# Optimization experiments

Measured on AMD Instinct MI355X. Metric: run time of the kernel, lower is better.

The kernel has to match this reference:

```python
import jax, jax.numpy as jnp
import numpy as np

H, D = 2, 128            # heads, per-head dim
F_OUT = H * D            # out_channels = 256
N_ADD = 20000
N_DEL = 20000
E = 200000
N_SEL = 4096


def setup_inputs() -> dict:
    key = jax.random.key(0)
    ks = jax.random.split(key, 24)
    p = lambda k, shp: (jax.random.normal(k, shp, dtype=jnp.float32) * 0.05)
    inp = {
        "x_add": jax.random.normal(ks[0], (N_ADD, 768), dtype=jnp.float32),
        "x_del": jax.random.normal(ks[1], (N_DEL, 768), dtype=jnp.float32),
        # per-node-type projections (torch Linear: W [out,in], b [out])
        "W_add": p(ks[2], (F_OUT, 768)), "b_add": p(ks[3], (F_OUT,)),
        "W_del": p(ks[4], (F_OUT, 768)), "b_del": p(ks[5], (F_OUT,)),
        # per-edge-type attention vectors [H, D]
        "att_ad_s": p(ks[6], (H, D)), "att_ad_d": p(ks[7], (H, D)),
        "att_da_s": p(ks[8], (H, D)), "att_da_d": p(ks[9], (H, D)),
        "att_aa_s": p(ks[10], (H, D)), "att_aa_d": p(ks[11], (H, D)),
        "att_dd_s": p(ks[12], (H, D)), "att_dd_d": p(ks[13], (H, D)),
        # semantic attention: k_lin Linear(F_OUT->F_OUT) and query q [F_OUT]
        "k_W": p(ks[14], (F_OUT, F_OUT)), "k_b": p(ks[15], (F_OUT,)),
        "q": p(ks[16], (F_OUT,)),
        # edge indices: row 0 = src node ids, row 1 = dst node ids
        "ei_ad": jax.random.randint(ks[17], (2, E), 0, N_ADD),
        "ei_da": jax.random.randint(ks[18], (2, E), 0, N_DEL),
        "ei_aa": jax.random.randint(ks[19], (2, E), 0, N_ADD),
        "ei_dd": jax.random.randint(ks[20], (2, E), 0, N_DEL),
        "del_idx": jax.random.randint(ks[21], (N_SEL,), 0, N_DEL),
    }
    return inp


def _seg_softmax(a, seg, n):
    # numerically-stable softmax over edges grouped by destination node
    m = jax.ops.segment_max(a, seg, num_segments=n)
    m = jnp.where(jnp.isfinite(m), m, 0.0)
    e = jnp.exp(a - m[seg])
    s = jax.ops.segment_sum(e, seg, num_segments=n)
    return e / (s[seg] + 1e-16)


def _edge_attn(x_src, x_dst, att_s, att_d, ei, n_dst):
    # x_*: [N, H, D]; GAT-style additive attention with leaky_relu(0.2)
    a_s = (x_src * att_s).sum(-1)                   # [Ns, H]
    a_d = (x_dst * att_d).sum(-1)                   # [Nd, H]
    alpha = jax.nn.leaky_relu(a_s[ei[0]] + a_d[ei[1]], 0.2)  # [E, H]
    alpha = _seg_softmax(alpha, ei[1], n_dst)       # [E, H]
    msg = x_src[ei[0]] * alpha[:, :, None]          # [E, H, D]
    out = jax.ops.segment_sum(msg, ei[1], num_segments=n_dst)  # [Nd, H, D]
    return jax.nn.relu(out).reshape(n_dst, F_OUT)


def _group(xs, q, k_W, k_b):
    # semantic (metapath-level) attention
    out = jnp.stack(xs)                              # [M, N, F]
    score = (q * jnp.tanh(out @ k_W.T + k_b).mean(axis=1)).sum(-1)  # [M]
    attn = jax.nn.softmax(score)
    return (attn[:, None, None] * out).sum(0)        # [N, F]


def reference(x_add, x_del, W_add, b_add, W_del, b_del,
              att_ad_s, att_ad_d, att_da_s, att_da_d,
              att_aa_s, att_aa_d, att_dd_s, att_dd_d,
              k_W, k_b, q, ei_ad, ei_da, ei_aa, ei_dd, del_idx):
    ha = (x_add @ W_add.T + b_add).reshape(N_ADD, H, D)
    hd = (x_del @ W_del.T + b_del).reshape(N_DEL, H, D)
    # messages grouped by destination node type
    out_del_ad = _edge_attn(ha, hd, att_ad_s, att_ad_d, ei_ad, N_DEL)
    out_del_dd = _edge_attn(hd, hd, att_dd_s, att_dd_d, ei_dd, N_DEL)
    out_add_da = _edge_attn(hd, ha, att_da_s, att_da_d, ei_da, N_ADD)
    out_add_aa = _edge_attn(ha, ha, att_aa_s, att_aa_d, ei_aa, N_ADD)
    out_del = _group([out_del_ad, out_del_dd], q, k_W, k_b)
    _ = _group([out_add_da, out_add_aa], q, k_W, k_b)  # computed by HANConv, unused downstream
    return out_del[del_idx]  # index_select on del_node
```

## Files before the change

kernel.cpp:

```cpp
#include <hip/hip_runtime.h>
#include <hip/hip_bf16.h>


typedef unsigned short u16;
typedef __attribute__((ext_vector_type(8))) __bf16 bf16x8;
typedef __attribute__((ext_vector_type(4))) float f32x4;
typedef const __attribute__((address_space(1))) unsigned int* gu32p;
typedef __attribute__((address_space(3))) unsigned int* su32p;

#define CAP 48

__device__ inline float bf2f(u16 u) {
    union { unsigned int i; float f; } c; c.i = ((unsigned int)u) << 16; return c.f;
}
__device__ inline u16 f2bf(float f) {
    union { float f; unsigned int i; } c; c.f = f;
    return (u16)((c.i + 0x7fffu + ((c.i >> 16) & 1u)) >> 16);
}
__device__ inline bf16x8 cvt8(f32x4 a, f32x4 b) {
    bf16x8 r;
    r[0] = (__bf16)a[0]; r[1] = (__bf16)a[1]; r[2] = (__bf16)a[2]; r[3] = (__bf16)a[3];
    r[4] = (__bf16)b[0]; r[5] = (__bf16)b[1]; r[6] = (__bf16)b[2]; r[7] = (__bf16)b[3];
    return r;
}
__device__ inline float fast_tanh(float x) {
    x = fminf(9.f, fmaxf(-9.f, x));
    float t = __expf(2.f * x);
    return (t - 1.f) / (t + 1.f);
}

__global__ __launch_bounds__(256) void prep_fill(const float* __restrict__ W0, u16* __restrict__ wb0,
                                                 const float* __restrict__ W1, u16* __restrict__ wb1,
                                                 const float* __restrict__ kW, u16* __restrict__ kwb,
                                                 const int* __restrict__ eiA, int* __restrict__ cntA,
                                                 int* __restrict__ srcsA,
                                                 const int* __restrict__ eiB, int* __restrict__ cntB,
                                                 int* __restrict__ srcsB, int E) {
    int b = blockIdx.x;
    if (b < 224) {
        int idx = b * 256 + threadIdx.x;
        const float* s; u16* d; int i;
        if (idx < 24576)      { s = W0; d = wb0; i = idx; }
        else if (idx < 49152) { s = W1; d = wb1; i = idx - 24576; }
        else                  { s = kW; d = kwb; i = idx - 49152; }
        int e = i * 8;
        *(bf16x8*)(d + e) = cvt8(*(const f32x4*)(s + e), *(const f32x4*)(s + e + 4));
    } else {
        int idx = (b - 224) * 256 + threadIdx.x;
        int which = idx >= E;
        int e = idx - (which ? E : 0);
        if (e >= E) return;
        const int* ei = which ? eiB : eiA;
        int* cnt = which ? cntB : cntA;
        int* srcs = which ? srcsB : srcsA;
        int s = ei[e], d = ei[E + e];
        int slot = atomicAdd(&cnt[d], 1);
        if (slot < CAP) srcs[d * CAP + slot] = s;
    }
}

__global__ __launch_bounds__(512, 4) void gemm_h3(
    const float* __restrict__ X0, const u16* __restrict__ Wb0,
    const float* __restrict__ b0, u16* __restrict__ H0,
    const float* __restrict__ X1, const u16* __restrict__ Wb1,
    const float* __restrict__ b1, u16* __restrict__ H1,
    const float* __restrict__ w_ads, const float* __restrict__ w_add,
    const float* __restrict__ w_dds, const float* __restrict__ w_ddd,
    float* __restrict__ as_ad, float* __restrict__ ad_ad,
    float* __restrict__ as_dd, float* __restrict__ ad_dd, int M) {
    __shared__ u16 lds[40960];
    int id = blockIdx.x;
    int which = id >= 313;
    int bm = which ? id - 313 : id;
    const float* X = which ? X1 : X0;
    const u16* Wb = which ? Wb1 : Wb0;
    const float* bias = which ? b1 : b0;
    u16* H = which ? H1 : H0;

    int tid = threadIdx.x;
    int w = tid >> 6, lane = tid & 63;
    int wrow = w & 1, wcol = w >> 1;
    int row16 = lane & 15, quad = lane >> 4;

#define ISSUE_B(kt, slot) { \
    _Pragma("unroll") \
    for (int j = 0; j < 2; ++j) { \
        int rloc = (w * 2 + j) * 16 + (lane >> 2); \
        int cc = (lane & 3) ^ ((rloc >> 1) & 3); \
        const u16* gp = Wb + (size_t)rloc * 768 + (kt) * 32 + cc * 8; \
        u16* lp = lds + 16384 + (slot) * 8192 + (w * 2 + j) * 512; \
        __builtin_amdgcn_global_load_lds((gu32p)(const void*)gp, (su32p)(void*)lp, 16, 0, 0); \
    } }

#define ALOAD(c, ar) { \
    _Pragma("unroll") \
    for (int i = 0; i < 4; ++i) { \
        int idx = i * 512 + tid; \
        int row = idx >> 5, col4 = idx & 31; \
        int rg = bm * 64 + row; if (rg > M - 1) rg = M - 1; \
        ar[i] = *(const f32x4*)(X + (size_t)rg * 768 + (c) * 128 + col4 * 4); \
    } }

#define AWRITE(c, ar) { \
    _Pragma("unroll") \
    for (int i = 0; i < 4; ++i) { \
        int idx = i * 512 + tid; \
        int row = idx >> 5, col4 = idx & 31; \
        int off = ((c) & 1) * 8192 + row * 128 + (((col4 >> 1) ^ (row & 7)) << 3) + ((col4 & 1) << 2); \
        ushort4 v; v.x = f2bf(ar[i][0]); v.y = f2bf(ar[i][1]); v.z = f2bf(ar[i][2]); v.w = f2bf(ar[i][3]); \
        *(ushort4*)(lds + off) = v; \
    } }

#define STEP(ks) { \
    const int ksl = (ks) & 3, buf = ((ks) >> 2) & 1, slot = (ks) % 3; \
    bf16x8 af[2], bv[4]; \
    _Pragma("unroll") \
    for (int mi = 0; mi < 2; ++mi) { \
        int r = wrow * 32 + mi * 16 + row16; \
        af[mi] = *(const bf16x8*)(lds + buf * 8192 + r * 128 + (((ksl * 4 + quad) ^ (r & 7)) << 3)); \
    } \
    _Pragma("unroll") \
    for (int ni = 0; ni < 4; ++ni) { \
        int r = wcol * 64 + ni * 16 + row16; \
        bv[ni] = *(const bf16x8*)(lds + 16384 + slot * 8192 + r * 32 + ((quad ^ ((r >> 1) & 3)) << 3)); \
    } \
    _Pragma("unroll") \
    for (int mi = 0; mi < 2; ++mi) \
        _Pragma("unroll") \
        for (int ni = 0; ni < 4; ++ni) \
            acc[mi][ni] = __builtin_amdgcn_mfma_f32_16x16x32_bf16(af[mi], bv[ni], acc[mi][ni], 0, 0, 0); \
}

    f32x4 a0[4], a1[4];
    ISSUE_B(0, 0)
    ISSUE_B(1, 1)
    ALOAD(0, a0)
    ALOAD(1, a1)
    asm volatile("s_waitcnt vmcnt(4)" ::: "memory");
    AWRITE(0, a0)
    asm volatile("s_waitcnt lgkmcnt(0)" ::: "memory");
    asm volatile("s_barrier" ::: "memory");

    f32x4 acc[2][4] = {};
#pragma unroll
    for (int ks = 0; ks < 24; ++ks) {
        if (ks > 0) {
            const int wv = (ks == 23) ? 0 : (ks >= 17) ? 2 : ((ks & 2) ? 6 : 2);
            if (wv == 0)      asm volatile("s_waitcnt vmcnt(0) lgkmcnt(0)" ::: "memory");
            else if (wv == 2) asm volatile("s_waitcnt vmcnt(2) lgkmcnt(0)" ::: "memory");
            else              asm volatile("s_waitcnt vmcnt(6) lgkmcnt(0)" ::: "memory");
            asm volatile("s_barrier" ::: "memory");
        }
        if (ks < 22) ISSUE_B(ks + 2, (ks + 2) % 3)
        if (ks == 0) {
            asm volatile("s_waitcnt vmcnt(2)" ::: "memory");
            AWRITE(1, a1)
        } else if ((ks & 3) == 0 && ks <= 16) {
            AWRITE(ks / 4 + 1, a0)
        }
        if ((ks & 3) == 1 && ks <= 13) ALOAD(ks / 4 + 2, a0)
        STEP(ks)
    }
#undef ISSUE_B
#undef ALOAD
#undef AWRITE
#undef STEP

    __syncthreads();
    u16* eps = lds;
    const int SE2 = 264;
#pragma unroll
    for (int mi = 0; mi < 2; ++mi)
#pragma unroll
        for (int ni = 0; ni < 4; ++ni) {
            int col = wcol * 64 + ni * 16 + row16;
            float bvv = bias[col];
#pragma unroll
            for (int r = 0; r < 4; ++r)
                eps[(wrow * 32 + mi * 16 + quad * 4 + r) * SE2 + col] = f2bf(acc[mi][ni][r] + bvv);
        }
    __syncthreads();
    int mlim = M - bm * 64;
    int c0 = (tid & 31) * 8;
    int hh = c0 >> 7;
    float wv0[8], wv1[8], wv2[8];
    const float* att0 = which ? w_add : w_ads;
#pragma unroll
    for (int j = 0; j < 8; ++j) {
        wv0[j] = att0[c0 + j];
        wv1[j] = w_dds[c0 + j];
        wv2[j] = w_ddd[c0 + j];
    }
#pragma unroll
    for (int p = 0; p < 4; ++p) {
        int row = p * 16 + (tid >> 5);
        union { uint4 q; u16 s[8]; } v;
        v.q = *(const uint4*)(eps + row * SE2 + c0);
        if (row < mlim)
            *(uint4*)(H + (size_t)(bm * 64 + row) * 256 + c0) = v.q;
        float d0 = 0.f, d1 = 0.f, d2 = 0.f;
#pragma unroll
        for (int j = 0; j < 8; ++j) {
            float hv = bf2f(v.s[j]);
            d0 += hv * wv0[j];
            if (which) { d1 += hv * wv1[j]; d2 += hv * wv2[j]; }
        }
#pragma unroll
        for (int off = 8; off >= 1; off >>= 1) {
            d0 += __shfl_down(d0, off, 16);
            if (which) { d1 += __shfl_down(d1, off, 16); d2 += __shfl_down(d2, off, 16); }
        }
        if ((tid & 15) == 0 && row < mlim) {
            int n = bm * 64 + row;
            if (!which) {
                unsafeAtomicAdd(&as_ad[n * 2 + hh], d0);
            } else {
                unsafeAtomicAdd(&ad_ad[n * 2 + hh], d0);
                unsafeAtomicAdd(&as_dd[n * 2 + hh], d1);
                unsafeAtomicAdd(&ad_dd[n * 2 + hh], d2);
            }
        }
    }
}

__global__ __launch_bounds__(256) void edge_gather4(const int* __restrict__ cntA, const int* __restrict__ srcsA,
                                                    const float* __restrict__ asA, const float* __restrict__ adA,
                                                    const u16* __restrict__ hA, u16* __restrict__ outA,
                                                    const int* __restrict__ cntB, const int* __restrict__ srcsB,
                                                    const float* __restrict__ asB, const float* __restrict__ adB,
                                                    const u16* __restrict__ hB, u16* __restrict__ outB, int N) {
    int gid = blockIdx.x * 256 + threadIdx.x;
    int grp = gid >> 5;
    int which = grp >= N;
    int d = grp - (which ? N : 0);
    if (d >= N) return;
    const int* cnt = which ? cntB : cntA;
    const int* srcs = which ? srcsB : srcsA;
    const float* a_src = which ? asB : asA;
    const float* a_dst = which ? adB : adA;
    const u16* h = which ? hB : hA;
    u16* out = which ? outB : outA;
    int l = gid & 31;
    int hh = l >> 4;
    int f = l * 8;
    float ad0 = a_dst[d * 2 + hh];
    int deg = cnt[d]; if (deg > CAP) deg = CAP;
    const int* sp = srcs + d * CAP;
    float acc[8] = {0.f, 0.f, 0.f, 0.f, 0.f, 0.f, 0.f, 0.f};
    float S = 0.f;
    union U8 { uint4 q; u16 s[8]; };
    int p = 0;
    for (; p + 4 <= deg; p += 4) {
        int4 s4 = *(const int4*)(sp + p);
        U8 x0, x1, x2, x3;
        x0.q = *(const uint4*)(h + (size_t)s4.x * 256 + f);
        x1.q = *(const uint4*)(h + (size_t)s4.y * 256 + f);
        x2.q = *(const uint4*)(h + (size_t)s4.z * 256 + f);
        x3.q = *(const uint4*)(h + (size_t)s4.w * 256 + f);
        float v0 = a_src[s4.x * 2 + hh] + ad0;
        float v1 = a_src[s4.y * 2 + hh] + ad0;
        float v2 = a_src[s4.z * 2 + hh] + ad0;
        float v3 = a_src[s4.w * 2 + hh] + ad0;
        v0 = v0 > 0.f ? v0 : 0.2f * v0;
        v1 = v1 > 0.f ? v1 : 0.2f * v1;
        v2 = v2 > 0.f ? v2 : 0.2f * v2;
        v3 = v3 > 0.f ? v3 : 0.2f * v3;
        float e0 = __expf(v0), e1 = __expf(v1), e2 = __expf(v2), e3 = __expf(v3);
        S += (e0 + e1) + (e2 + e3);
#pragma unroll
        for (int j = 0; j < 8; ++j)
            acc[j] += e0 * bf2f(x0.s[j]) + e1 * bf2f(x1.s[j]) + e2 * bf2f(x2.s[j]) + e3 * bf2f(x3.s[j]);
    }
    for (; p < deg; ++p) {
        int s0 = sp[p];
        U8 x0; x0.q = *(const uint4*)(h + (size_t)s0 * 256 + f);
        float v0 = a_src[s0 * 2 + hh] + ad0;
        v0 = v0 > 0.f ? v0 : 0.2f * v0;
        float e0 = __expf(v0);
        S += e0;
#pragma unroll
        for (int j = 0; j < 8; ++j) acc[j] += e0 * bf2f(x0.s[j]);
    }
    float inv = 1.f / (S + 1e-16f);
    union U8 o;
#pragma unroll
    for (int j = 0; j < 8; ++j) o.s[j] = f2bf(acc[j] * inv);
    *(uint4*)(out + (size_t)d * 256 + f) = o.q;
}

#define SK 264
__global__ __launch_bounds__(256) void kgemm_score2(const u16* __restrict__ outA,
                                                    const u16* __restrict__ outB,
                                                    const u16* __restrict__ kwb,
                                                    const float* __restrict__ kb,
                                                    const float* __restrict__ qv,
                                                    float* __restrict__ score) {
    __shared__ u16 Bs[128 * SK];
    __shared__ float red[4];
    int slot = blockIdx.x >> 8;
    int b = blockIdx.x & 255;
    const u16* outm = slot ? outB : outA;
    int bn = b & 1;
    int bidx = b >> 1;
    int tid = threadIdx.x;
    int w = tid >> 6, lane = tid & 63;
    int row16 = lane & 15, quad = lane >> 4;

#pragma unroll
    for (int i = 0; i < 16; ++i) {
        int c = tid + 256 * i;
        int r = c >> 5, col8 = (c & 31) * 8;
        *(bf16x8*)(Bs + r * SK + col8) = *(const bf16x8*)(kwb + (size_t)(bn * 128 + r) * 256 + col8);
    }
    __syncthreads();

    float kb0 = kb[bn * 128 + w * 32 + row16];
    float qn0 = qv[bn * 128 + w * 32 + row16];
    float kb1 = kb[bn * 128 + w * 32 + 16 + row16];
    float qn1 = qv[bn * 128 + w * 32 + 16 + row16];
    const u16* b0 = Bs + (w * 32 + row16) * SK + quad * 8;
    const u16* b1 = Bs + (w * 32 + 16 + row16) * SK + quad * 8;

    union U { uint4 q; unsigned int u[4]; u16 s[8]; bf16x8 v; };
    float p = 0.f;
    for (int mt = bidx; mt < 1250; mt += 128) {
        const u16* arow = outm + (size_t)(mt * 16 + row16) * 256 + quad * 8;
        U a[8];
#pragma unroll
        for (int s8 = 0; s8 < 8; ++s8) a[s8].q = *(const uint4*)(arow + s8 * 32);
        f32x4 acc0 = {0.f,0.f,0.f,0.f}, acc1 = {0.f,0.f,0.f,0.f};
#pragma unroll
        for (int s8 = 0; s8 < 8; ++s8) {
#pragma unroll
            for (int u = 0; u < 4; ++u) {
                unsigned int x = a[s8].u[u];
                unsigned int sg = x & 0x80008000u;
                unsigned int m = sg | (sg - (sg >> 15));
                a[s8].u[u] = x & ~m;
            }
            bf16x8 bf0 = *(const bf16x8*)(b0 + s8 * 32);
            bf16x8 bf1 = *(const bf16x8*)(b1 + s8 * 32);
            acc0 = __builtin_amdgcn_mfma_f32_16x16x32_bf16(a[s8].v, bf0, acc0, 0, 0, 0);
            acc1 = __builtin_amdgcn_mfma_f32_16x16x32_bf16(a[s8].v, bf1, acc1, 0, 0, 0);
        }
#pragma unroll
        for (int r = 0; r < 4; ++r) {
            p += qn0 * fast_tanh(acc0[r] + kb0);
            p += qn1 * fast_tanh(acc1[r] + kb1);
        }
    }
#pragma unroll
    for (int off = 32; off >= 1; off >>= 1) p += __shfl_down(p, off, 64);
    if (lane == 0) red[w] = p;
    __syncthreads();
    if (tid == 0) unsafeAtomicAdd(&score[slot], red[0] + red[1] + red[2] + red[3]);
}

__global__ __launch_bounds__(256) void final_combine(const u16* __restrict__ out_ad,
                                                     const u16* __restrict__ out_dd,
                                                     const float* __restrict__ score,
                                                     const int* __restrict__ del_idx,
                                                     float* __restrict__ out) {
    int i = blockIdx.x;
    int f = threadIdx.x;
    int node = del_idx[i];
    float s0 = score[0] * (1.f / 20000.f);
    float s1 = score[1] * (1.f / 20000.f);
    float m = fmaxf(s0, s1);
    float e0 = __expf(s0 - m), e1 = __expf(s1 - m);
    float inv = 1.f / (e0 + e1);
    float a0 = e0 * inv, a1 = e1 * inv;
    float v0 = bf2f(out_ad[(size_t)node * 256 + f]); v0 = v0 > 0.f ? v0 : 0.f;
    float v1 = bf2f(out_dd[(size_t)node * 256 + f]); v1 = v1 > 0.f ? v1 : 0.f;
    out[(size_t)i * 256 + f] = a0 * v0 + a1 * v1;
}

extern "C" void kernel_launch(void* const* d_in, const int* in_sizes, int n_in,
                              void* d_out, int out_size, void* d_ws, size_t ws_size,
                              hipStream_t stream) {
    const float* x_add    = (const float*)d_in[0];
    const float* x_del    = (const float*)d_in[1];
    const float* W_add    = (const float*)d_in[2];
    const float* b_add    = (const float*)d_in[3];
    const float* W_del    = (const float*)d_in[4];
    const float* b_del    = (const float*)d_in[5];
    const float* att_ad_s = (const float*)d_in[6];
    const float* att_ad_d = (const float*)d_in[7];
    const float* att_dd_s = (const float*)d_in[12];
    const float* att_dd_d = (const float*)d_in[13];
    const float* k_W      = (const float*)d_in[14];
    const float* k_b      = (const float*)d_in[15];
    const float* q        = (const float*)d_in[16];
    const int* ei_ad      = (const int*)d_in[17];
    const int* ei_dd      = (const int*)d_in[20];
    const int* del_idx    = (const int*)d_in[21];
    float* out = (float*)d_out;

    const int N = 20000, E = 200000;
    char* ws = (char*)d_ws;
    size_t o = 0;
    int* cnt_ad = (int*)(ws + o); o += (size_t)N * 4;
    int* cnt_dd = (int*)(ws + o); o += (size_t)N * 4;
    float* as_ad = (float*)(ws + o); o += (size_t)N * 2 * 4;
    float* ad_ad = (float*)(ws + o); o += (size_t)N * 2 * 4;
    float* as_dd = (float*)(ws + o); o += (size_t)N * 2 * 4;
    float* ad_dd = (float*)(ws + o); o += (size_t)N * 2 * 4;
    float* score = (float*)(ws + o); o += 256;
    size_t zero_bytes = o;
    u16* wb_add = (u16*)(ws + o); o += (size_t)256 * 768 * 2;
    u16* wb_del = (u16*)(ws + o); o += (size_t)256 * 768 * 2;
    u16* kwb    = (u16*)(ws + o); o += (size_t)256 * 256 * 2;
    int* srcs_ad = (int*)(ws + o); o += (size_t)N * CAP * 4;
    int* srcs_dd = (int*)(ws + o); o += (size_t)N * CAP * 4;
    u16* out_ad = (u16*)(ws + o); o += (size_t)N * 256 * 2;
    u16* out_dd = (u16*)(ws + o); o += (size_t)N * 256 * 2;
    u16* ha    = (u16*)(ws + o); o += (size_t)N * 256 * 2;
    u16* hd    = (u16*)(ws + o); o += (size_t)N * 256 * 2;

    hipMemsetAsync(d_ws, 0, zero_bytes, stream);

    prep_fill<<<224 + (2 * E + 255) / 256, 256, 0, stream>>>(
        W_add, wb_add, W_del, wb_del, k_W, kwb,
        ei_ad, cnt_ad, srcs_ad, ei_dd, cnt_dd, srcs_dd, E);

    gemm_h3<<<626, 512, 0, stream>>>(x_add, wb_add, b_add, ha,
                                     x_del, wb_del, b_del, hd,
                                     att_ad_s, att_ad_d, att_dd_s, att_dd_d,
                                     as_ad, ad_ad, as_dd, ad_dd, N);

    edge_gather4<<<(2 * N * 32 + 255) / 256, 256, 0, stream>>>(
        cnt_ad, srcs_ad, as_ad, ad_ad, ha, out_ad,
        cnt_dd, srcs_dd, as_dd, ad_dd, hd, out_dd, N);

    kgemm_score2<<<512, 256, 0, stream>>>(out_ad, out_dd, kwb, k_b, q, score);
    final_combine<<<4096, 256, 0, stream>>>(out_ad, out_dd, score, del_idx, out);
}
```

Measured before the change: 290.2 us.

## Double GEMM M-tile to 128 rows and pad edge-gather tail into vector loop

The projection GEMM now gives each block 128 rows with a K-slice of 64. Each wave holds a 4x4 accumulator tile, the grid shrinks from 626 to 314 blocks, and the A-staging and waitcnt schedule is rebuilt around the new slice size. The intent is more reuse of each B tile and fewer blocks, at the cost of more registers per wave and fewer blocks to balance across CUs. The edge gather drops its scalar remainder loop: tail lanes duplicate the first source and get zero weight, which keeps every step in the 4-wide loop but spends extra loads on padding.

```diff
diff --git a/kernel.cpp b/kernel.cpp
--- a/kernel.cpp
+++ b/kernel.cpp
@@ -59,7 +59,7 @@
     }
 }
 
-__global__ __launch_bounds__(512, 4) void gemm_h3(
+__global__ __launch_bounds__(512, 4) void gemm_h4(
     const float* __restrict__ X0, const u16* __restrict__ Wb0,
     const float* __restrict__ b0, u16* __restrict__ H0,
     const float* __restrict__ X1, const u16* __restrict__ Wb1,
@@ -70,8 +70,8 @@
     float* __restrict__ as_dd, float* __restrict__ ad_dd, int M) {
     __shared__ u16 lds[40960];
     int id = blockIdx.x;
-    int which = id >= 313;
-    int bm = which ? id - 313 : id;
+    int which = id >= 157;
+    int bm = which ? id - 157 : id;
     const float* X = which ? X1 : X0;
     const u16* Wb = which ? Wb1 : Wb0;
     const float* bias = which ? b1 : b0;
@@ -79,7 +79,7 @@
 
     int tid = threadIdx.x;
     int w = tid >> 6, lane = tid & 63;
-    int wrow = w & 1, wcol = w >> 1;
+    int wr = w & 1, wc = w >> 1;
     int row16 = lane & 15, quad = lane >> 4;
 
 #define ISSUE_B(kt, slot) { \
@@ -96,69 +96,71 @@
     _Pragma("unroll") \
     for (int i = 0; i < 4; ++i) { \
         int idx = i * 512 + tid; \
-        int row = idx >> 5, col4 = idx & 31; \
-        int rg = bm * 64 + row; if (rg > M - 1) rg = M - 1; \
-        ar[i] = *(const f32x4*)(X + (size_t)rg * 768 + (c) * 128 + col4 * 4); \
+        int row = idx >> 4, col4 = idx & 15; \
+        int rg = bm * 128 + row; if (rg > M - 1) rg = M - 1; \
+        ar[i] = *(const f32x4*)(X + (size_t)rg * 768 + (c) * 64 + col4 * 4); \
     } }
 
 #define AWRITE(c, ar) { \
     _Pragma("unroll") \
     for (int i = 0; i < 4; ++i) { \
         int idx = i * 512 + tid; \
-        int row = idx >> 5, col4 = idx & 31; \
-        int off = ((c) & 1) * 8192 + row * 128 + (((col4 >> 1) ^ (row & 7)) << 3) + ((col4 & 1) << 2); \
+        int row = idx >> 4, col4 = idx & 15; \
+        int off = ((c) & 1) * 8192 + row * 64 + (((col4 >> 1) ^ (row & 7)) << 3) + ((col4 & 1) << 2); \
         ushort4 v; v.x = f2bf(ar[i][0]); v.y = f2bf(ar[i][1]); v.z = f2bf(ar[i][2]); v.w = f2bf(ar[i][3]); \
         *(ushort4*)(lds + off) = v; \
     } }
 
 #define STEP(ks) { \
-    const int ksl = (ks) & 3, buf = ((ks) >> 2) & 1, slot = (ks) % 3; \
-    bf16x8 af[2], bv[4]; \
-    _Pragma("unroll") \
-    for (int mi = 0; mi < 2; ++mi) { \
-        int r = wrow * 32 + mi * 16 + row16; \
-        af[mi] = *(const bf16x8*)(lds + buf * 8192 + r * 128 + (((ksl * 4 + quad) ^ (r & 7)) << 3)); \
+    const int ksl = (ks) & 1, buf = ((ks) >> 1) & 1, slot = (ks) % 3; \
+    bf16x8 af[4], bv[4]; \
+    _Pragma("unroll") \
+    for (int mi = 0; mi < 4; ++mi) { \
+        int r = wr * 64 + mi * 16 + row16; \
+        af[mi] = *(const bf16x8*)(lds + buf * 8192 + r * 64 + (((ksl * 4 + quad) ^ (r & 7)) << 3)); \
     } \
     _Pragma("unroll") \
     for (int ni = 0; ni < 4; ++ni) { \
-        int r = wcol * 64 + ni * 16 + row16; \
+        int r = wc * 64 + ni * 16 + row16; \
         bv[ni] = *(const bf16x8*)(lds + 16384 + slot * 8192 + r * 32 + ((quad ^ ((r >> 1) & 3)) << 3)); \
     } \
     _Pragma("unroll") \
-    for (int mi = 0; mi < 2; ++mi) \
+    for (int mi = 0; mi < 4; ++mi) \
         _Pragma("unroll") \
         for (int ni = 0; ni < 4; ++ni) \
             acc[mi][ni] = __builtin_amdgcn_mfma_f32_16x16x32_bf16(af[mi], bv[ni], acc[mi][ni], 0, 0, 0); \
 }
 
-    f32x4 a0[4], a1[4];
+    f32x4 a0[4];
     ISSUE_B(0, 0)
     ISSUE_B(1, 1)
     ALOAD(0, a0)
-    ALOAD(1, a1)
-    asm volatile("s_waitcnt vmcnt(4)" ::: "memory");
+    asm volatile("s_waitcnt vmcnt(0)" ::: "memory");
     AWRITE(0, a0)
+    ALOAD(1, a0)
     asm volatile("s_waitcnt lgkmcnt(0)" ::: "memory");
     asm volatile("s_barrier" ::: "memory");
 
-    f32x4 acc[2][4] = {};
+    f32x4 acc[4][4] = {};
 #pragma unroll
     for (int ks = 0; ks < 24; ++ks) {
         if (ks > 0) {
-            const int wv = (ks == 23) ? 0 : (ks >= 17) ? 2 : ((ks & 2) ? 6 : 2);
+            const int wv = (ks == 23) ? 0 : (ks >= 21) ? 2 : 6;
             if (wv == 0)      asm volatile("s_waitcnt vmcnt(0) lgkmcnt(0)" ::: "memory");
             else if (wv == 2) asm volatile("s_waitcnt vmcnt(2) lgkmcnt(0)" ::: "memory");
             else              asm volatile("s_waitcnt vmcnt(6) lgkmcnt(0)" ::: "memory");
             asm volatile("s_barrier" ::: "memory");
         }
         if (ks < 22) ISSUE_B(ks + 2, (ks + 2) % 3)
-        if (ks == 0) {
-            asm volatile("s_waitcnt vmcnt(2)" ::: "memory");
-            AWRITE(1, a1)
-        } else if ((ks & 3) == 0 && ks <= 16) {
-            AWRITE(ks / 4 + 1, a0)
-        }
-        if ((ks & 3) == 1 && ks <= 13) ALOAD(ks / 4 + 2, a0)
+        if ((ks & 1) == 0) {
+            const int t = ks >> 1;
+            if (t + 1 <= 11) {
+                if (ks == 0) asm volatile("s_waitcnt vmcnt(2)" ::: "memory");
+                else         asm volatile("s_waitcnt vmcnt(4)" ::: "memory");
+                AWRITE(t + 1, a0)
+            }
+            if (t + 2 <= 11) ALOAD(t + 2, a0)
+        }
         STEP(ks)
     }
 #undef ISSUE_B
@@ -170,17 +172,17 @@
     u16* eps = lds;
     const int SE2 = 264;
 #pragma unroll
-    for (int mi = 0; mi < 2; ++mi)
+    for (int mi = 0; mi < 4; ++mi)
 #pragma unroll
         for (int ni = 0; ni < 4; ++ni) {
-            int col = wcol * 64 + ni * 16 + row16;
+            int col = wc * 64 + ni * 16 + row16;
             float bvv = bias[col];
 #pragma unroll
             for (int r = 0; r < 4; ++r)
-                eps[(wrow * 32 + mi * 16 + quad * 4 + r) * SE2 + col] = f2bf(acc[mi][ni][r] + bvv);
+                eps[(wr * 64 + mi * 16 + quad * 4 + r) * SE2 + col] = f2bf(acc[mi][ni][r] + bvv);
         }
     __syncthreads();
-    int mlim = M - bm * 64;
+    int mlim = M - bm * 128;
     int c0 = (tid & 31) * 8;
     int hh = c0 >> 7;
     float wv0[8], wv1[8], wv2[8];
@@ -192,12 +194,12 @@
         wv2[j] = w_ddd[c0 + j];
     }
 #pragma unroll
-    for (int p = 0; p < 4; ++p) {
+    for (int p = 0; p < 8; ++p) {
         int row = p * 16 + (tid >> 5);
         union { uint4 q; u16 s[8]; } v;
         v.q = *(const uint4*)(eps + row * SE2 + c0);
         if (row < mlim)
-            *(uint4*)(H + (size_t)(bm * 64 + row) * 256 + c0) = v.q;
+            *(uint4*)(H + (size_t)(bm * 128 + row) * 256 + c0) = v.q;
         float d0 = 0.f, d1 = 0.f, d2 = 0.f;
 #pragma unroll
         for (int j = 0; j < 8; ++j) {
@@ -211,7 +213,7 @@
             if (which) { d1 += __shfl_down(d1, off, 16); d2 += __shfl_down(d2, off, 16); }
         }
         if ((tid & 15) == 0 && row < mlim) {
-            int n = bm * 64 + row;
+            int n = bm * 128 + row;
             if (!which) {
                 unsafeAtomicAdd(&as_ad[n * 2 + hh], d0);
             } else {
@@ -223,7 +225,7 @@
     }
 }
 
-__global__ __launch_bounds__(256) void edge_gather4(const int* __restrict__ cntA, const int* __restrict__ srcsA,
+__global__ __launch_bounds__(256) void edge_gather5(const int* __restrict__ cntA, const int* __restrict__ srcsA,
                                                     const float* __restrict__ asA, const float* __restrict__ adA,
                                                     const u16* __restrict__ hA, u16* __restrict__ outA,
                                                     const int* __restrict__ cntB, const int* __restrict__ srcsB,
@@ -249,37 +251,34 @@
     float acc[8] = {0.f, 0.f, 0.f, 0.f, 0.f, 0.f, 0.f, 0.f};
     float S = 0.f;
     union U8 { uint4 q; u16 s[8]; };
-    int p = 0;
-    for (; p + 4 <= deg; p += 4) {
+    int nb = (deg + 3) & ~3;
+    for (int p = 0; p < nb; p += 4) {
         int4 s4 = *(const int4*)(sp + p);
+        int s0 = s4.x;
+        int s1 = (p + 1 < deg) ? s4.y : s0;
+        int s2 = (p + 2 < deg) ? s4.z : s0;
+        int s3 = (p + 3 < deg) ? s4.w : s0;
         U8 x0, x1, x2, x3;
-        x0.q = *(const uint4*)(h + (size_t)s4.x * 256 + f);
-        x1.q = *(const uint4*)(h + (size_t)s4.y * 256 + f);
-        x2.q = *(const uint4*)(h + (size_t)s4.z * 256 + f);
-        x3.q = *(const uint4*)(h + (size_t)s4.w * 256 + f);
-        float v0 = a_src[s4.x * 2 + hh] + ad0;
-        float v1 = a_src[s4.y * 2 + hh] + ad0;
-        float v2 = a_src[s4.z * 2 + hh] + ad0;
-        float v3 = a_src[s4.w * 2 + hh] + ad0;
+        x0.q = *(const uint4*)(h + (size_t)s0 * 256 + f);
+        x1.q = *(const uint4*)(h + (size_t)s1 * 256 + f);
+        x2.q = *(const uint4*)(h + (size_t)s2 * 256 + f);
+        x3.q = *(const uint4*)(h + (size_t)s3 * 256 + f);
+        float v0 = a_src[s0 * 2 + hh] + ad0;
+        float v1 = a_src[s1 * 2 + hh] + ad0;
+        float v2 = a_src[s2 * 2 + hh] + ad0;
+        float v3 = a_src[s3 * 2 + hh] + ad0;
         v0 = v0 > 0.f ? v0 : 0.2f * v0;
         v1 = v1 > 0.f ? v1 : 0.2f * v1;
         v2 = v2 > 0.f ? v2 : 0.2f * v2;
         v3 = v3 > 0.f ? v3 : 0.2f * v3;
-        float e0 = __expf(v0), e1 = __expf(v1), e2 = __expf(v2), e3 = __expf(v3);
+        float e0 = __expf(v0);
+        float e1 = (p + 1 < deg) ? __expf(v1) : 0.f;
+        float e2 = (p + 2 < deg) ? __expf(v2) : 0.f;
+        float e3 = (p + 3 < deg) ? __expf(v3) : 0.f;
         S += (e0 + e1) + (e2 + e3);
 #pragma unroll
         for (int j = 0; j < 8; ++j)
             acc[j] += e0 * bf2f(x0.s[j]) + e1 * bf2f(x1.s[j]) + e2 * bf2f(x2.s[j]) + e3 * bf2f(x3.s[j]);
-    }
-    for (; p < deg; ++p) {
-        int s0 = sp[p];
-        U8 x0; x0.q = *(const uint4*)(h + (size_t)s0 * 256 + f);
-        float v0 = a_src[s0 * 2 + hh] + ad0;
-        v0 = v0 > 0.f ? v0 : 0.2f * v0;
-        float e0 = __expf(v0);
-        S += e0;
-#pragma unroll
-        for (int j = 0; j < 8; ++j) acc[j] += e0 * bf2f(x0.s[j]);
     }
     float inv = 1.f / (S + 1e-16f);
     union U8 o;
@@ -423,12 +422,12 @@
         W_add, wb_add, W_del, wb_del, k_W, kwb,
         ei_ad, cnt_ad, srcs_ad, ei_dd, cnt_dd, srcs_dd, E);
 
-    gemm_h3<<<626, 512, 0, stream>>>(x_add, wb_add, b_add, ha,
+    gemm_h4<<<314, 512, 0, stream>>>(x_add, wb_add, b_add, ha,
                                      x_del, wb_del, b_del, hd,
                                      att_ad_s, att_ad_d, att_dd_s, att_dd_d,
                                      as_ad, ad_ad, as_dd, ad_dd, N);
 
-    edge_gather4<<<(2 * N * 32 + 255) / 256, 256, 0, stream>>>(
+    edge_gather5<<<(2 * N * 32 + 255) / 256, 256, 0, stream>>>(
         cnt_ad, srcs_ad, as_ad, ad_ad, ha, out_ad,
         cnt_dd, srcs_dd, as_dd, ad_dd, hd, out_dd, N);
 
```

Result: slower. 321.7 us (+10.9%).

## Fuse edge gather, score GEMM and final combine into one persistent kernel

Applied to the files above, without the earlier changes.

Replaces three launches (edge aggregation, semantic-score GEMM, final combine) with one persistent kernel of 1024 blocks separated by software grid barriers built on atomic counters. The score GEMM now keeps k_W fragments in registers instead of shared memory, and the gather tail loop is folded into a padded 4-wide loop. This removes launch gaps and tail effects between stages, but relies on all 1024 blocks being co-resident, which could deadlock if occupancy is lower than assumed, and adds barrier spin cost.

```diff
diff --git a/kernel.cpp b/kernel.cpp
--- a/kernel.cpp
+++ b/kernel.cpp
@@ -9,6 +9,7 @@
 typedef __attribute__((address_space(3))) unsigned int* su32p;
 
 #define CAP 48
+#define GFT 1024
 
 __device__ inline float bf2f(u16 u) {
     union { unsigned int i; float f; } c; c.i = ((unsigned int)u) << 16; return c.f;
@@ -223,156 +224,163 @@
     }
 }
 
-__global__ __launch_bounds__(256) void edge_gather4(const int* __restrict__ cntA, const int* __restrict__ srcsA,
-                                                    const float* __restrict__ asA, const float* __restrict__ adA,
-                                                    const u16* __restrict__ hA, u16* __restrict__ outA,
-                                                    const int* __restrict__ cntB, const int* __restrict__ srcsB,
-                                                    const float* __restrict__ asB, const float* __restrict__ adB,
-                                                    const u16* __restrict__ hB, u16* __restrict__ outB, int N) {
-    int gid = blockIdx.x * 256 + threadIdx.x;
-    int grp = gid >> 5;
-    int which = grp >= N;
-    int d = grp - (which ? N : 0);
-    if (d >= N) return;
-    const int* cnt = which ? cntB : cntA;
-    const int* srcs = which ? srcsB : srcsA;
-    const float* a_src = which ? asB : asA;
-    const float* a_dst = which ? adB : adA;
-    const u16* h = which ? hB : hA;
-    u16* out = which ? outB : outA;
-    int l = gid & 31;
-    int hh = l >> 4;
-    int f = l * 8;
-    float ad0 = a_dst[d * 2 + hh];
-    int deg = cnt[d]; if (deg > CAP) deg = CAP;
-    const int* sp = srcs + d * CAP;
-    float acc[8] = {0.f, 0.f, 0.f, 0.f, 0.f, 0.f, 0.f, 0.f};
-    float S = 0.f;
-    union U8 { uint4 q; u16 s[8]; };
-    int p = 0;
-    for (; p + 4 <= deg; p += 4) {
-        int4 s4 = *(const int4*)(sp + p);
-        U8 x0, x1, x2, x3;
-        x0.q = *(const uint4*)(h + (size_t)s4.x * 256 + f);
-        x1.q = *(const uint4*)(h + (size_t)s4.y * 256 + f);
-        x2.q = *(const uint4*)(h + (size_t)s4.z * 256 + f);
-        x3.q = *(const uint4*)(h + (size_t)s4.w * 256 + f);
-        float v0 = a_src[s4.x * 2 + hh] + ad0;
-        float v1 = a_src[s4.y * 2 + hh] + ad0;
-        float v2 = a_src[s4.z * 2 + hh] + ad0;
-        float v3 = a_src[s4.w * 2 + hh] + ad0;
-        v0 = v0 > 0.f ? v0 : 0.2f * v0;
-        v1 = v1 > 0.f ? v1 : 0.2f * v1;
-        v2 = v2 > 0.f ? v2 : 0.2f * v2;
-        v3 = v3 > 0.f ? v3 : 0.2f * v3;
-        float e0 = __expf(v0), e1 = __expf(v1), e2 = __expf(v2), e3 = __expf(v3);
-        S += (e0 + e1) + (e2 + e3);
-#pragma unroll
-        for (int j = 0; j < 8; ++j)
-            acc[j] += e0 * bf2f(x0.s[j]) + e1 * bf2f(x1.s[j]) + e2 * bf2f(x2.s[j]) + e3 * bf2f(x3.s[j]);
-    }
-    for (; p < deg; ++p) {
-        int s0 = sp[p];
-        U8 x0; x0.q = *(const uint4*)(h + (size_t)s0 * 256 + f);
-        float v0 = a_src[s0 * 2 + hh] + ad0;
-        v0 = v0 > 0.f ? v0 : 0.2f * v0;
-        float e0 = __expf(v0);
-        S += e0;
-#pragma unroll
-        for (int j = 0; j < 8; ++j) acc[j] += e0 * bf2f(x0.s[j]);
-    }
-    float inv = 1.f / (S + 1e-16f);
-    union U8 o;
-#pragma unroll
-    for (int j = 0; j < 8; ++j) o.s[j] = f2bf(acc[j] * inv);
-    *(uint4*)(out + (size_t)d * 256 + f) = o.q;
-}
-
-#define SK 264
-__global__ __launch_bounds__(256) void kgemm_score2(const u16* __restrict__ outA,
-                                                    const u16* __restrict__ outB,
-                                                    const u16* __restrict__ kwb,
-                                                    const float* __restrict__ kb,
-                                                    const float* __restrict__ qv,
-                                                    float* __restrict__ score) {
-    __shared__ u16 Bs[128 * SK];
+__device__ inline void gbar(int* cnt, int* gen) {
+    __syncthreads();
+    if (threadIdx.x == 0) {
+        __threadfence();
+        if (atomicAdd(cnt, 1) == GFT - 1) {
+            atomicAdd(gen, 1);
+        } else {
+            while (atomicAdd(gen, 0) == 0) __builtin_amdgcn_s_sleep(8);
+        }
+        __threadfence();
+    }
+    __syncthreads();
+}
+
+__global__ __launch_bounds__(256, 4) void fused_tail(
+    const int* __restrict__ cntA, const int* __restrict__ srcsA,
+    const float* __restrict__ asA, const float* __restrict__ adA,
+    const u16* __restrict__ hA, u16* __restrict__ outA,
+    const int* __restrict__ cntB, const int* __restrict__ srcsB,
+    const float* __restrict__ asB, const float* __restrict__ adB,
+    const u16* __restrict__ hB, u16* __restrict__ outB,
+    const u16* __restrict__ kwb, const float* __restrict__ kb,
+    const float* __restrict__ qv, float* __restrict__ score,
+    const int* __restrict__ del_idx, float* __restrict__ outF,
+    int* __restrict__ bar, int N) {
     __shared__ float red[4];
-    int slot = blockIdx.x >> 8;
-    int b = blockIdx.x & 255;
-    const u16* outm = slot ? outB : outA;
-    int bn = b & 1;
-    int bidx = b >> 1;
     int tid = threadIdx.x;
-    int w = tid >> 6, lane = tid & 63;
-    int row16 = lane & 15, quad = lane >> 4;
-
-#pragma unroll
-    for (int i = 0; i < 16; ++i) {
-        int c = tid + 256 * i;
-        int r = c >> 5, col8 = (c & 31) * 8;
-        *(bf16x8*)(Bs + r * SK + col8) = *(const bf16x8*)(kwb + (size_t)(bn * 128 + r) * 256 + col8);
-    }
-    __syncthreads();
-
-    float kb0 = kb[bn * 128 + w * 32 + row16];
-    float qn0 = qv[bn * 128 + w * 32 + row16];
-    float kb1 = kb[bn * 128 + w * 32 + 16 + row16];
-    float qn1 = qv[bn * 128 + w * 32 + 16 + row16];
-    const u16* b0 = Bs + (w * 32 + row16) * SK + quad * 8;
-    const u16* b1 = Bs + (w * 32 + 16 + row16) * SK + quad * 8;
-
-    union U { uint4 q; unsigned int u[4]; u16 s[8]; bf16x8 v; };
-    float p = 0.f;
-    for (int mt = bidx; mt < 1250; mt += 128) {
-        const u16* arow = outm + (size_t)(mt * 16 + row16) * 256 + quad * 8;
-        U a[8];
-#pragma unroll
-        for (int s8 = 0; s8 < 8; ++s8) a[s8].q = *(const uint4*)(arow + s8 * 32);
-        f32x4 acc0 = {0.f,0.f,0.f,0.f}, acc1 = {0.f,0.f,0.f,0.f};
+
+    {
+        int l = tid & 31;
+        int hh = l >> 4;
+        int f = l * 8;
+        for (int gbase = blockIdx.x * 8; gbase < 2 * N; gbase += GFT * 8) {
+            int grp = gbase + (tid >> 5);
+            int which = grp >= N;
+            int d = grp - (which ? N : 0);
+            if (d >= N) continue;
+            const int* cnt = which ? cntB : cntA;
+            const int* srcs = which ? srcsB : srcsA;
+            const float* a_src = which ? asB : asA;
+            const float* a_dst = which ? adB : adA;
+            const u16* h = which ? hB : hA;
+            u16* out = which ? outB : outA;
+            float ad0 = a_dst[d * 2 + hh];
+            int deg = cnt[d]; if (deg > CAP) deg = CAP;
+            const int* sp = srcs + d * CAP;
+            float acc[8] = {0.f, 0.f, 0.f, 0.f, 0.f, 0.f, 0.f, 0.f};
+            float S = 0.f;
+            union U8 { uint4 q; u16 s[8]; };
+            int nb = (deg + 3) & ~3;
+            for (int p = 0; p < nb; p += 4) {
+                int4 s4 = *(const int4*)(sp + p);
+                int s0 = s4.x;
+                int s1 = (p + 1 < deg) ? s4.y : s0;
+                int s2 = (p + 2 < deg) ? s4.z : s0;
+                int s3 = (p + 3 < deg) ? s4.w : s0;
+                U8 x0, x1, x2, x3;
+                x0.q = *(const uint4*)(h + (size_t)s0 * 256 + f);
+                x1.q = *(const uint4*)(h + (size_t)s1 * 256 + f);
+                x2.q = *(const uint4*)(h + (size_t)s2 * 256 + f);
+                x3.q = *(const uint4*)(h + (size_t)s3 * 256 + f);
+                float v0 = a_src[s0 * 2 + hh] + ad0;
+                float v1 = a_src[s1 * 2 + hh] + ad0;
+                float v2 = a_src[s2 * 2 + hh] + ad0;
+                float v3 = a_src[s3 * 2 + hh] + ad0;
+                v0 = v0 > 0.f ? v0 : 0.2f * v0;
+                v1 = v1 > 0.f ? v1 : 0.2f * v1;
+                v2 = v2 > 0.f ? v2 : 0.2f * v2;
+                v3 = v3 > 0.f ? v3 : 0.2f * v3;
+                float e0 = __expf(v0);
+                float e1 = (p + 1 < deg) ? __expf(v1) : 0.f;
+                float e2 = (p + 2 < deg) ? __expf(v2) : 0.f;
+                float e3 = (p + 3 < deg) ? __expf(v3) : 0.f;
+                S += (e0 + e1) + (e2 + e3);
+#pragma unroll
+                for (int j = 0; j < 8; ++j)
+                    acc[j] += e0 * bf2f(x0.s[j]) + e1 * bf2f(x1.s[j]) + e2 * bf2f(x2.s[j]) + e3 * bf2f(x3.s[j]);
+            }
+            float inv = 1.f / (S + 1e-16f);
+            union U8 o;
+#pragma unroll
+            for (int j = 0; j < 8; ++j) o.s[j] = f2bf(acc[j] * inv);
+            *(uint4*)(out + (size_t)d * 256 + f) = o.q;
+        }
+    }
+
+    gbar(&bar[0], &bar[1]);
+
+    {
+        int slot = blockIdx.x >> 9;
+        int b = blockIdx.x & 511;
+        const u16* outm = slot ? outB : outA;
+        int bn = b & 1;
+        int bidx = b >> 1;
+        int w = tid >> 6, lane = tid & 63;
+        int row16 = lane & 15, quad = lane >> 4;
+        int r0 = bn * 128 + w * 32 + row16;
+        int r1 = r0 + 16;
+        float kb0 = kb[r0], qn0 = qv[r0];
+        float kb1 = kb[r1], qn1 = qv[r1];
+        bf16x8 b0r[8], b1r[8];
 #pragma unroll
         for (int s8 = 0; s8 < 8; ++s8) {
-#pragma unroll
-            for (int u = 0; u < 4; ++u) {
-                unsigned int x = a[s8].u[u];
-                unsigned int sg = x & 0x80008000u;
-                unsigned int m = sg | (sg - (sg >> 15));
-                a[s8].u[u] = x & ~m;
+            b0r[s8] = *(const bf16x8*)(kwb + (size_t)r0 * 256 + quad * 8 + s8 * 32);
+            b1r[s8] = *(const bf16x8*)(kwb + (size_t)r1 * 256 + quad * 8 + s8 * 32);
+        }
+        union U { uint4 q; unsigned int u[4]; u16 s[8]; bf16x8 v; };
+        float p = 0.f;
+        for (int mt = bidx; mt < 1250; mt += 256) {
+            const u16* arow = outm + (size_t)(mt * 16 + row16) * 256 + quad * 8;
+            U a[8];
+#pragma unroll
+            for (int s8 = 0; s8 < 8; ++s8) a[s8].q = *(const uint4*)(arow + s8 * 32);
+            f32x4 acc0 = {0.f,0.f,0.f,0.f}, acc1 = {0.f,0.f,0.f,0.f};
+#pragma unroll
+            for (int s8 = 0; s8 < 8; ++s8) {
+#pragma unroll
+                for (int u = 0; u < 4; ++u) {
+                    unsigned int x = a[s8].u[u];
+                    unsigned int sg = x & 0x80008000u;
+                    unsigned int m = sg | (sg - (sg >> 15));
+                    a[s8].u[u] = x & ~m;
+                }
+                acc0 = __builtin_amdgcn_mfma_f32_16x16x32_bf16(a[s8].v, b0r[s8], acc0, 0, 0, 0);
+                acc1 = __builtin_amdgcn_mfma_f32_16x16x32_bf16(a[s8].v, b1r[s8], acc1, 0, 0, 0);
             }
-            bf16x8 bf0 = *(const bf16x8*)(b0 + s8 * 32);
-            bf16x8 bf1 = *(const bf16x8*)(b1 + s8 * 32);
-            acc0 = __builtin_amdgcn_mfma_f32_16x16x32_bf16(a[s8].v, bf0, acc0, 0, 0, 0);
-            acc1 = __builtin_amdgcn_mfma_f32_16x16x32_bf16(a[s8].v, bf1, acc1, 0, 0, 0);
-        }
-#pragma unroll
-        for (int r = 0; r < 4; ++r) {
-            p += qn0 * fast_tanh(acc0[r] + kb0);
-            p += qn1 * fast_tanh(acc1[r] + kb1);
-        }
-    }
-#pragma unroll
-    for (int off = 32; off >= 1; off >>= 1) p += __shfl_down(p, off, 64);
-    if (lane == 0) red[w] = p;
-    __syncthreads();
-    if (tid == 0) unsafeAtomicAdd(&score[slot], red[0] + red[1] + red[2] + red[3]);
-}
-
-__global__ __launch_bounds__(256) void final_combine(const u16* __restrict__ out_ad,
-                                                     const u16* __restrict__ out_dd,
-                                                     const float* __restrict__ score,
-                                                     const int* __restrict__ del_idx,
-                                                     float* __restrict__ out) {
-    int i = blockIdx.x;
-    int f = threadIdx.x;
-    int node = del_idx[i];
-    float s0 = score[0] * (1.f / 20000.f);
-    float s1 = score[1] * (1.f / 20000.f);
-    float m = fmaxf(s0, s1);
-    float e0 = __expf(s0 - m), e1 = __expf(s1 - m);
-    float inv = 1.f / (e0 + e1);
-    float a0 = e0 * inv, a1 = e1 * inv;
-    float v0 = bf2f(out_ad[(size_t)node * 256 + f]); v0 = v0 > 0.f ? v0 : 0.f;
-    float v1 = bf2f(out_dd[(size_t)node * 256 + f]); v1 = v1 > 0.f ? v1 : 0.f;
-    out[(size_t)i * 256 + f] = a0 * v0 + a1 * v1;
+#pragma unroll
+            for (int r = 0; r < 4; ++r) {
+                p += qn0 * fast_tanh(acc0[r] + kb0);
+                p += qn1 * fast_tanh(acc1[r] + kb1);
+            }
+        }
+#pragma unroll
+        for (int off = 32; off >= 1; off >>= 1) p += __shfl_down(p, off, 64);
+        if (lane == 0) red[w] = p;
+        __syncthreads();
+        if (tid == 0) unsafeAtomicAdd(&score[slot], red[0] + red[1] + red[2] + red[3]);
+    }
+
+    gbar(&bar[2], &bar[3]);
+
+    {
+        float s0 = score[0] * (1.f / 20000.f);
+        float s1 = score[1] * (1.f / 20000.f);
+        float m = fmaxf(s0, s1);
+        float e0 = __expf(s0 - m), e1 = __expf(s1 - m);
+        float inv = 1.f / (e0 + e1);
+        float a0 = e0 * inv, a1 = e1 * inv;
+        int gtid = blockIdx.x * 256 + tid;
+        for (int e = gtid; e < 4096 * 256; e += GFT * 256) {
+            int i = e >> 8, fcol = e & 255;
+            int node = del_idx[i];
+            float v0 = bf2f(outA[(size_t)node * 256 + fcol]); v0 = v0 > 0.f ? v0 : 0.f;
+            float v1 = bf2f(outB[(size_t)node * 256 + fcol]); v1 = v1 > 0.f ? v1 : 0.f;
+            outF[(size_t)i * 256 + fcol] = a0 * v0 + a1 * v1;
+        }
+    }
 }
 
 extern "C" void kernel_launch(void* const* d_in, const int* in_sizes, int n_in,
@@ -406,6 +414,7 @@
     float* as_dd = (float*)(ws + o); o += (size_t)N * 2 * 4;
     float* ad_dd = (float*)(ws + o); o += (size_t)N * 2 * 4;
     float* score = (float*)(ws + o); o += 256;
+    int* bar = (int*)(ws + o); o += 256;
     size_t zero_bytes = o;
     u16* wb_add = (u16*)(ws + o); o += (size_t)256 * 768 * 2;
     u16* wb_del = (u16*)(ws + o); o += (size_t)256 * 768 * 2;
@@ -428,10 +437,8 @@
                                      att_ad_s, att_ad_d, att_dd_s, att_dd_d,
                                      as_ad, ad_ad, as_dd, ad_dd, N);
 
-    edge_gather4<<<(2 * N * 32 + 255) / 256, 256, 0, stream>>>(
+    fused_tail<<<GFT, 256, 0, stream>>>(
         cnt_ad, srcs_ad, as_ad, ad_ad, ha, out_ad,
-        cnt_dd, srcs_dd, as_dd, ad_dd, hd, out_dd, N);
-
-    kgemm_score2<<<512, 256, 0, stream>>>(out_ad, out_dd, kwb, k_b, q, score);
-    final_combine<<<4096, 256, 0, stream>>>(out_ad, out_dd, score, del_idx, out);
-}
+        cnt_dd, srcs_dd, as_dd, ad_dd, hd, out_dd,
+        kwb, k_b, q, score, del_idx, out, bar, N);
+}
```

Result: slower. 526.9 us (+81.5%).
